# Kernel optimization log

Measured on AMD Instinct MI355X. Metric: run time of the kernel, lower is better.

Reference implementation:

```python
import jax, jax.numpy as jnp
import numpy as np

B, T, D, N = 8, 2048, 1024, 256


def setup_inputs() -> dict:
    key = jax.random.key(0)
    ks = jax.random.split(key, 6)
    sD = 1.0 / np.sqrt(D)
    sN = 1.0 / np.sqrt(N)
    return {
        "x": jax.random.normal(ks[0], (B, T, D), dtype=jnp.float32),
        "Wa": jax.random.normal(ks[1], (D, N), dtype=jnp.float32) * sD,
        "ba": jnp.zeros((N,), jnp.float32),
        "Wb": jax.random.normal(ks[2], (D, N), dtype=jnp.float32) * sD,
        "bb": jnp.zeros((N,), jnp.float32),
        "Wc": jax.random.normal(ks[3], (D, N), dtype=jnp.float32) * sD,
        "bc": jnp.zeros((N,), jnp.float32),
        "Wd": jax.random.normal(ks[4], (D, D), dtype=jnp.float32) * sD,
        "bd": jnp.zeros((D,), jnp.float32),
        "Wy": jax.random.normal(ks[5], (N, D), dtype=jnp.float32) * sN,
        "by": jnp.zeros((D,), jnp.float32),
    }


def reference(x, Wa, ba, Wb, bb, Wc, bc, Wd, bd, Wy, by):
    # Precompute all input-dependent gates/projections in batched GEMMs.
    a = jax.nn.sigmoid(jnp.einsum("btd,dn->btn", x, Wa) + ba)  # (B,T,N)
    b = jnp.einsum("btd,dn->btn", x, Wb) + bb                   # (B,T,N)
    c = jnp.tanh(jnp.einsum("btd,dn->btn", x, Wc) + bc)          # (B,T,N)
    d = jnp.einsum("btd,de->bte", x, Wd) + bd                    # (B,T,D)

    # Sequential linear-gated recurrence: s_t = a_t*s_{t-1} + (1-a_t)*b_t
    def step(s, abc):
        at, bt, ct = abc
        s = at * s + (1.0 - at) * bt
        return s, ct * s

    aT = jnp.swapaxes(a, 0, 1)  # (T,B,N)
    bT = jnp.swapaxes(b, 0, 1)
    cT = jnp.swapaxes(c, 0, 1)
    s0 = jnp.zeros((x.shape[0], Wa.shape[1]), x.dtype)
    _, csT = jax.lax.scan(step, s0, (aT, bT, cT))  # (T,B,N)
    cs = jnp.swapaxes(csT, 0, 1)                    # (B,T,N)

    # Output projection applied once over the full sequence.
    y = jnp.einsum("btn,nd->btd", cs, Wy) + by + d  # (B,T,D)
    return y
```

## Files before the change

### kernel.cpp

```cpp
#include <hip/hip_runtime.h>
#include <hip/hip_bf16.h>

typedef unsigned short u16;
typedef __attribute__((ext_vector_type(8))) short bf16x8;
typedef __attribute__((ext_vector_type(4))) float f32x4;

#define AS1 __attribute__((address_space(1)))
#define AS3 __attribute__((address_space(3)))

#define Bx 8
#define Tt 2048
#define Dd 1024
#define Nn 256
#define Mm (Bx*Tt)
#define CHAINS (Bx*Nn)
#define NCH 32
#define TC 64
#define NCOMB 1792

__device__ __forceinline__ u16 f2bf(float f) {
  union { float f; unsigned u; } v; v.f = f;
  unsigned u = v.u;
  u += 0x7fffu + ((u >> 16) & 1u);
  return (u16)(u >> 16);
}

__device__ __forceinline__ void gload_lds16(const void* g, void* l) {
  __builtin_amdgcn_global_load_lds((AS1 void*)(g), (AS3 void*)(l), 16, 0, 0);
}

__global__ void cvt_x_kernel(const float* __restrict__ x, u16* __restrict__ xb) {
  int i = blockIdx.x * blockDim.x + threadIdx.x;
  float4 v = ((const float4*)x)[i];
  unsigned lo = (unsigned)f2bf(v.x) | ((unsigned)f2bf(v.y) << 16);
  unsigned hi = (unsigned)f2bf(v.z) | ((unsigned)f2bf(v.w) << 16);
  ((uint2*)xb)[i] = make_uint2(lo, hi);
}

__global__ void pack_w_kernel(const float* __restrict__ Wa, const float* __restrict__ Wb,
                              const float* __restrict__ Wc, const float* __restrict__ Wd,
                              const float* __restrict__ Wy,
                              u16* __restrict__ Wcomb, u16* __restrict__ Wyt) {
  __shared__ float tile[32][33];
  int z = blockIdx.z;
  const float* src; u16* dst; int R, C, dld;
  if (z < 3)       { src = (z==0?Wa:(z==1?Wb:Wc)); dst = Wcomb + (size_t)z*256*1024; R=1024; C=256;  dld=1024; }
  else if (z == 3) { src = Wd; dst = Wcomb + (size_t)768*1024; R=1024; C=1024; dld=1024; }
  else             { src = Wy; dst = Wyt; R=256;  C=1024; dld=256;  }
  int c0 = blockIdx.x * 32, r0 = blockIdx.y * 32;
  if (c0 >= C || r0 >= R) return;
  int tx = threadIdx.x & 31, ty = threadIdx.x >> 5;
  #pragma unroll
  for (int i = 0; i < 32; i += 8)
    tile[ty + i][tx] = src[(size_t)(r0 + ty + i)*C + (c0 + tx)];
  __syncthreads();
  #pragma unroll
  for (int i = 0; i < 32; i += 8) {
    int c = c0 + ty + i, r = r0 + tx;
    dst[(size_t)c*dld + r] = f2bf(tile[tx][ty + i]);
  }
}

template<int EPI>
__global__ __launch_bounds__(256) void gemm_bt_kernel(
    const u16* __restrict__ A, const u16* __restrict__ Bt, int K,
    float* __restrict__ outA, float* __restrict__ outO,
    const float* __restrict__ b0, const float* __restrict__ b1,
    const float* __restrict__ b2, const float* __restrict__ b3) {
  __shared__ u16 ldsA[128*64];
  __shared__ u16 ldsB[128*64];
  const int tid = threadIdx.x;
  const int lane = tid & 63, wid = tid >> 6;
  const int wr = wid >> 1, wc = wid & 1;
  const int m0 = blockIdx.y * 128, n0 = blockIdx.x * 128;

  f32x4 acc[4][4] = {};

  const int srow = lane >> 3;
  const int sq   = (lane & 7) ^ srow;
  const char* Ab = (const char*)A;
  const char* Bb = (const char*)Bt;

  const int kq  = lane >> 4;
  const int swz = lane & 7;
  const int arow = wr*64 + (lane & 15);
  const int brow = wc*64 + (lane & 15);

  for (int k0 = 0; k0 < K; k0 += 64) {
    #pragma unroll
    for (int i = 0; i < 4; ++i) {
      int g = wid*4 + i;
      int r = g*8 + srow;
      gload_lds16(Ab + ((size_t)(m0 + r)*K + k0 + sq*8)*2, (char*)ldsA + g*1024);
      gload_lds16(Bb + ((size_t)(n0 + r)*K + k0 + sq*8)*2, (char*)ldsB + g*1024);
    }
    __syncthreads();
    #pragma unroll
    for (int kk = 0; kk < 2; ++kk) {
      const int q = ((kk*4 + kq) ^ swz) * 8;
      bf16x8 af[4], bfr[4];
      #pragma unroll
      for (int mi = 0; mi < 4; ++mi)
        af[mi]  = *(const bf16x8*)&ldsA[(arow + mi*16)*64 + q];
      #pragma unroll
      for (int ni = 0; ni < 4; ++ni)
        bfr[ni] = *(const bf16x8*)&ldsB[(brow + ni*16)*64 + q];
      #pragma unroll
      for (int mi = 0; mi < 4; ++mi)
        #pragma unroll
        for (int ni = 0; ni < 4; ++ni)
          acc[mi][ni] = __builtin_amdgcn_mfma_f32_16x16x32_bf16(af[mi], bfr[ni], acc[mi][ni], 0, 0, 0);
    }
    __syncthreads();
  }

  const int crow = m0 + wr*64 + (lane >> 4)*4;
  const int ccol = wc*64 + (lane & 15);
  #pragma unroll
  for (int mi = 0; mi < 4; ++mi) {
    #pragma unroll
    for (int ni = 0; ni < 4; ++ni) {
      int coln = n0 + ccol + ni*16;
      #pragma unroll
      for (int r = 0; r < 4; ++r) {
        int row = crow + mi*16 + r;
        float v = acc[mi][ni][r];
        if (EPI == 0) {
          if (n0 < 768) {
            int seg = coln >> 8, cn = coln & 255;
            if (seg == 0)      v = 1.f / (1.f + __expf(-(v + b0[cn])));
            else if (seg == 1) v = v + b1[cn];
            else               v = tanhf(v + b2[cn]);
            outA[(size_t)row*768 + coln] = v;
          } else {
            int col = coln - 768;
            outO[(size_t)row*1024 + col] = v + b3[col];
          }
        } else {
          outO[(size_t)row*1024 + coln] += v + b0[coln];
        }
      }
    }
  }
}

__global__ void scanA_kernel(const float* __restrict__ abc,
                             float* __restrict__ Asum, float* __restrict__ Usum) {
  int idx = blockIdx.x * blockDim.x + threadIdx.x;
  int chain = idx & (CHAINS - 1);
  int ch = idx >> 11;
  int bb = chain >> 8, n = chain & 255;
  const float* base = abc + (size_t)(bb*Tt + ch*TC) * 768;
  float A = 1.f, U = 0.f;
  for (int t = 0; t < TC; ++t) {
    float a = base[(size_t)t*768 + n];
    float b = base[(size_t)t*768 + 256 + n];
    U = a*U + (1.f - a)*b;
    A *= a;
  }
  Asum[idx] = A; Usum[idx] = U;
}

__global__ void scanB_kernel(const float* __restrict__ Asum, const float* __restrict__ Usum,
                             float* __restrict__ Spre) {
  int chain = blockIdx.x * blockDim.x + threadIdx.x;
  float s = 0.f;
  for (int ch = 0; ch < NCH; ++ch) {
    int i = (ch << 11) + chain;
    Spre[i] = s;
    s = Asum[i]*s + Usum[i];
  }
}

__global__ void scanC_kernel(const float* __restrict__ abc, const float* __restrict__ Spre,
                             u16* __restrict__ cs) {
  int idx = blockIdx.x * blockDim.x + threadIdx.x;
  int chain = idx & (CHAINS - 1);
  int ch = idx >> 11;
  int bb = chain >> 8, n = chain & 255;
  const float* base = abc + (size_t)(bb*Tt + ch*TC) * 768;
  u16* csb = cs + (size_t)(bb*Tt + ch*TC) * 256 + n;
  float s = Spre[idx];
  for (int t = 0; t < TC; ++t) {
    float a = base[(size_t)t*768 + n];
    float b = base[(size_t)t*768 + 256 + n];
    float c = base[(size_t)t*768 + 512 + n];
    s = a*s + (1.f - a)*b;
    csb[(size_t)t*256] = f2bf(c*s);
  }
}

extern "C" void kernel_launch(void* const* d_in, const int* in_sizes, int n_in,
                              void* d_out, int out_size, void* d_ws, size_t ws_size,
                              hipStream_t stream) {
  const float* x  = (const float*)d_in[0];
  const float* Wa = (const float*)d_in[1];
  const float* ba = (const float*)d_in[2];
  const float* Wb = (const float*)d_in[3];
  const float* bb = (const float*)d_in[4];
  const float* Wc = (const float*)d_in[5];
  const float* bc = (const float*)d_in[6];
  const float* Wd = (const float*)d_in[7];
  const float* bd = (const float*)d_in[8];
  const float* Wy = (const float*)d_in[9];
  const float* by = (const float*)d_in[10];
  float* out = (float*)d_out;
  char* ws = (char*)d_ws;

  u16*  xb    = (u16*) (ws + 0);
  u16*  Wcomb = (u16*) (ws + 33554432);
  u16*  Wyt   = (u16*) (ws + 37224448);
  float* abc  = (float*)(ws + 37748736);
  u16*  cs    = (u16*) (ws + 88080384);
  float* Asum = (float*)(ws + 96468992);
  float* Usum = (float*)(ws + 96731136);
  float* Spre = (float*)(ws + 96993280);

  cvt_x_kernel<<<Mm*Dd/4/256, 256, 0, stream>>>(x, xb);
  pack_w_kernel<<<dim3(32, 32, 5), 256, 0, stream>>>(Wa, Wb, Wc, Wd, Wy, Wcomb, Wyt);
  gemm_bt_kernel<0><<<dim3(NCOMB/128, Mm/128), 256, 0, stream>>>(
      xb, Wcomb, Dd, abc, out, ba, bb, bc, bd);
  scanA_kernel<<<CHAINS*NCH/256, 256, 0, stream>>>(abc, Asum, Usum);
  scanB_kernel<<<CHAINS/256, 256, 0, stream>>>(Asum, Usum, Spre);
  scanC_kernel<<<CHAINS*NCH/256, 256, 0, stream>>>(abc, Spre, cs);
  gemm_bt_kernel<2><<<dim3(Dd/128, Mm/128), 256, 0, stream>>>(
      cs, Wyt, Nn, nullptr, out, by, nullptr, nullptr, nullptr);
}
```

Baseline: 183.5 us.

## Replace GEMM with 256x256 double-buffered 8-wave pipelined kernel

Replaces the 128x128 single-buffered GEMM with a 256x256 tile, 512-thread kernel that uses 128KB of dynamic LDS for double buffering. Global-to-LDS loads for the next K step are interleaved with MFMA quarter-tiles under explicit vmcnt waits, barriers and setprio, so memory traffic overlaps compute. A block-ID remap groups tiles for better L2 reuse. This adds register pressure and barrier overhead, and with 128KB of LDS per block the __launch_bounds__(512,2) occupancy target may not be reached.

```diff
diff --git a/kernel.cpp b/kernel.cpp
--- a/kernel.cpp
+++ b/kernel.cpp
@@ -17,6 +17,11 @@
 #define NCH 32
 #define TC 64
 #define NCOMB 1792
+
+#define VMCNT4 asm volatile("s_waitcnt vmcnt(4)" ::: "memory")
+#define VMCNT0 asm volatile("s_waitcnt vmcnt(0)" ::: "memory")
+#define BARR   __builtin_amdgcn_s_barrier()
+#define SCHEDB __builtin_amdgcn_sched_barrier(0)
 
 __device__ __forceinline__ u16 f2bf(float f) {
   union { float f; unsigned u; } v; v.f = f;
@@ -62,83 +67,141 @@
 }
 
 template<int EPI>
-__global__ __launch_bounds__(256) void gemm_bt_kernel(
-    const u16* __restrict__ A, const u16* __restrict__ Bt, int K,
+__global__ __launch_bounds__(512, 2) void gemm8p_kernel(
+    const u16* __restrict__ A, const u16* __restrict__ Bt, int K, int gx,
     float* __restrict__ outA, float* __restrict__ outO,
     const float* __restrict__ b0, const float* __restrict__ b1,
     const float* __restrict__ b2, const float* __restrict__ b3) {
-  __shared__ u16 ldsA[128*64];
-  __shared__ u16 ldsB[128*64];
-  const int tid = threadIdx.x;
+  extern __shared__ u16 lds[];
+  const int tid  = threadIdx.x;
   const int lane = tid & 63, wid = tid >> 6;
-  const int wr = wid >> 1, wc = wid & 1;
-  const int m0 = blockIdx.y * 128, n0 = blockIdx.x * 128;
-
-  f32x4 acc[4][4] = {};
-
-  const int srow = lane >> 3;
-  const int sq   = (lane & 7) ^ srow;
-  const char* Ab = (const char*)A;
-  const char* Bb = (const char*)Bt;
-
-  const int kq  = lane >> 4;
-  const int swz = lane & 7;
-  const int arow = wr*64 + (lane & 15);
-  const int brow = wc*64 + (lane & 15);
-
-  for (int k0 = 0; k0 < K; k0 += 64) {
-    #pragma unroll
-    for (int i = 0; i < 4; ++i) {
-      int g = wid*4 + i;
-      int r = g*8 + srow;
-      gload_lds16(Ab + ((size_t)(m0 + r)*K + k0 + sq*8)*2, (char*)ldsA + g*1024);
-      gload_lds16(Bb + ((size_t)(n0 + r)*K + k0 + sq*8)*2, (char*)ldsB + g*1024);
-    }
-    __syncthreads();
-    #pragma unroll
-    for (int kk = 0; kk < 2; ++kk) {
-      const int q = ((kk*4 + kq) ^ swz) * 8;
-      bf16x8 af[4], bfr[4];
-      #pragma unroll
-      for (int mi = 0; mi < 4; ++mi)
-        af[mi]  = *(const bf16x8*)&ldsA[(arow + mi*16)*64 + q];
-      #pragma unroll
-      for (int ni = 0; ni < 4; ++ni)
-        bfr[ni] = *(const bf16x8*)&ldsB[(brow + ni*16)*64 + q];
+  const int wm = wid >> 2, wn = wid & 3;
+
+  const int nwg = gridDim.x;
+  const int h   = blockIdx.x;
+  const int id  = (h & 7) * (nwg >> 3) + (h >> 3);
+  const int mt  = id / gx, nt = id % gx;
+  const int m0  = mt * 256, n0 = nt * 256;
+  const int NT  = K >> 6;
+
+  const int rl  = tid >> 3;
+  const int ssl = (tid & 7) ^ (rl & 7);
+
+  const int lr = lane & 15, kq = lane >> 4, sw = lane & 7;
+
+  auto stA = [&](int q, int bn, int kn) {
+    gload_lds16(A + (size_t)(m0 + q*64 + rl)*K + kn + ssl*8,
+                lds + bn*16384 + q*4096 + wid*512);
+  };
+  auto stB = [&](int q, int bn, int kn) {
+    gload_lds16(Bt + (size_t)(n0 + q*64 + rl)*K + kn + ssl*8,
+                lds + 32768 + bn*16384 + q*4096 + wid*512);
+  };
+  auto rdA = [&](int buf, int row, int kk) -> bf16x8 {
+    return *(const bf16x8*)(lds + buf*16384 + row*64 + (((kk*4 + kq) ^ sw) << 3));
+  };
+  auto rdB = [&](int buf, int row, int kk) -> bf16x8 {
+    return *(const bf16x8*)(lds + 32768 + buf*16384 + row*64 + (((kk*4 + kq) ^ sw) << 3));
+  };
+
+  f32x4 acc[2][2][4][2] = {};
+
+  auto mma8 = [&](f32x4 (&ac)[4][2], const bf16x8 (&af)[4][2], const bf16x8 (&bf)[2][2]) {
+    __builtin_amdgcn_s_setprio(1);
+    #pragma unroll
+    for (int kk = 0; kk < 2; ++kk)
       #pragma unroll
       for (int mi = 0; mi < 4; ++mi)
         #pragma unroll
-        for (int ni = 0; ni < 4; ++ni)
-          acc[mi][ni] = __builtin_amdgcn_mfma_f32_16x16x32_bf16(af[mi], bfr[ni], acc[mi][ni], 0, 0, 0);
-    }
-    __syncthreads();
-  }
-
-  const int crow = m0 + wr*64 + (lane >> 4)*4;
-  const int ccol = wc*64 + (lane & 15);
-  #pragma unroll
-  for (int mi = 0; mi < 4; ++mi) {
-    #pragma unroll
-    for (int ni = 0; ni < 4; ++ni) {
-      int coln = n0 + ccol + ni*16;
-      #pragma unroll
-      for (int r = 0; r < 4; ++r) {
-        int row = crow + mi*16 + r;
-        float v = acc[mi][ni][r];
-        if (EPI == 0) {
-          if (n0 < 768) {
-            int seg = coln >> 8, cn = coln & 255;
-            if (seg == 0)      v = 1.f / (1.f + __expf(-(v + b0[cn])));
-            else if (seg == 1) v = v + b1[cn];
-            else               v = tanhf(v + b2[cn]);
-            outA[(size_t)row*768 + coln] = v;
-          } else {
-            int col = coln - 768;
-            outO[(size_t)row*1024 + col] = v + b3[col];
-          }
+        for (int ni = 0; ni < 2; ++ni)
+          ac[mi][ni] = __builtin_amdgcn_mfma_f32_16x16x32_bf16(af[mi][kk], bf[ni][kk], ac[mi][ni], 0, 0, 0);
+    __builtin_amdgcn_s_setprio(0);
+  };
+
+  stA(0,0,0); stA(1,0,0); stB(0,0,0); stB(1,0,0);
+  stB(2,0,0); stB(3,0,0); stA(2,0,0); stA(3,0,0);
+  VMCNT4;
+  BARR; SCHEDB;
+
+  for (int t = 0; t < NT; ++t) {
+    const int buf = t & 1, bn = buf ^ 1;
+    const int kn = (t + 1 < NT) ? (t + 1) << 6 : 0;
+    bf16x8 a0f[4][2], a1f[4][2], b0f[2][2], b1f[2][2];
+
+    #pragma unroll
+    for (int mi = 0; mi < 4; ++mi) {
+      a0f[mi][0] = rdA(buf, wm*64 + mi*16 + lr, 0);
+      a0f[mi][1] = rdA(buf, wm*64 + mi*16 + lr, 1);
+    }
+    #pragma unroll
+    for (int ni = 0; ni < 2; ++ni) {
+      b0f[ni][0] = rdB(buf, wn*32 + ni*16 + lr, 0);
+      b0f[ni][1] = rdB(buf, wn*32 + ni*16 + lr, 1);
+    }
+    stA(0, bn, kn); stA(1, bn, kn);
+    VMCNT4;
+    BARR;
+    mma8(acc[0][0], a0f, b0f);
+    BARR; SCHEDB;
+
+    #pragma unroll
+    for (int ni = 0; ni < 2; ++ni) {
+      b1f[ni][0] = rdB(buf, 128 + wn*32 + ni*16 + lr, 0);
+      b1f[ni][1] = rdB(buf, 128 + wn*32 + ni*16 + lr, 1);
+    }
+    stB(0, bn, kn); stB(1, bn, kn);
+    VMCNT4;
+    BARR;
+    mma8(acc[0][1], a0f, b1f);
+    BARR; SCHEDB;
+
+    #pragma unroll
+    for (int mi = 0; mi < 4; ++mi) {
+      a1f[mi][0] = rdA(buf, 128 + wm*64 + mi*16 + lr, 0);
+      a1f[mi][1] = rdA(buf, 128 + wm*64 + mi*16 + lr, 1);
+    }
+    stB(2, bn, kn); stB(3, bn, kn);
+    BARR;
+    mma8(acc[1][0], a1f, b0f);
+    BARR; SCHEDB;
+
+    stA(2, bn, kn); stA(3, bn, kn);
+    VMCNT4;
+    BARR;
+    mma8(acc[1][1], a1f, b1f);
+    BARR; SCHEDB;
+  }
+  VMCNT0;
+
+  const int orow = (lane >> 4) * 4;
+  const int ocol = lane & 15;
+  #pragma unroll
+  for (int mq = 0; mq < 2; ++mq)
+  #pragma unroll
+  for (int nq = 0; nq < 2; ++nq)
+  #pragma unroll
+  for (int mi = 0; mi < 4; ++mi)
+  #pragma unroll
+  for (int ni = 0; ni < 2; ++ni) {
+    const int rowb = m0 + mq*128 + wm*64 + mi*16 + orow;
+    const int coln = n0 + nq*128 + wn*32 + ni*16 + ocol;
+    #pragma unroll
+    for (int r = 0; r < 4; ++r) {
+      const int row = rowb + r;
+      float v = acc[mq][nq][mi][ni][r];
+      if (EPI == 0) {
+        if (coln < 768) {
+          const int seg = coln >> 8, cn = coln & 255;
+          if (seg == 0)      v = 1.f / (1.f + __expf(-(v + b0[cn])));
+          else if (seg == 1) v = v + b1[cn];
+          else               v = tanhf(v + b2[cn]);
+          outA[(size_t)row*768 + coln] = v;
         } else {
-          outO[(size_t)row*1024 + coln] += v + b0[coln];
+          const int col = coln - 768;
+          outO[(size_t)row*1024 + col] = v + b3[col];
         }
+      } else {
+        outO[(size_t)row*1024 + coln] += v + b0[coln];
       }
     }
   }
@@ -218,11 +281,11 @@
 
   cvt_x_kernel<<<Mm*Dd/4/256, 256, 0, stream>>>(x, xb);
   pack_w_kernel<<<dim3(32, 32, 5), 256, 0, stream>>>(Wa, Wb, Wc, Wd, Wy, Wcomb, Wyt);
-  gemm_bt_kernel<0><<<dim3(NCOMB/128, Mm/128), 256, 0, stream>>>(
-      xb, Wcomb, Dd, abc, out, ba, bb, bc, bd);
+  gemm8p_kernel<0><<<448, 512, 131072, stream>>>(
+      xb, Wcomb, Dd, NCOMB/256, abc, out, ba, bb, bc, bd);
   scanA_kernel<<<CHAINS*NCH/256, 256, 0, stream>>>(abc, Asum, Usum);
   scanB_kernel<<<CHAINS/256, 256, 0, stream>>>(Asum, Usum, Spre);
   scanC_kernel<<<CHAINS*NCH/256, 256, 0, stream>>>(abc, Spre, cs);
-  gemm_bt_kernel<2><<<dim3(Dd/128, Mm/128), 256, 0, stream>>>(
-      cs, Wyt, Nn, nullptr, out, by, nullptr, nullptr, nullptr);
-}
+  gemm8p_kernel<2><<<256, 512, 131072, stream>>>(
+      cs, Wyt, Nn, Dd/256, nullptr, out, by, nullptr, nullptr, nullptr);
+}
```

New measurement: 209.6 us. +14.2%, slower.
